# Performance work log

Measured on AMD Instinct MI355X. Metric: run time of the kernel, lower is better.

## Reference

```python
import jax, jax.numpy as jnp
import numpy as np

N, C, H, W = 4, 256, 64, 64
K = 4096

def setup_inputs() -> dict:
    key = jax.random.key(0)
    ks = jax.random.split(key, 9)
    bound = 1.0 / np.sqrt(C)  # torch Linear default init scale
    inp = {
        "latent0": jax.random.normal(ks[0], (N, C, H, W), dtype=jnp.float32),
        "code0": jax.random.randint(ks[1], (N, H, W), 0, K, dtype=jnp.int32).astype(jnp.int64),
        "codebook0": jax.random.normal(ks[2], (K, C), dtype=jnp.float32) * np.sqrt(2.0 / C),  # kaiming-ish
        "Wq": jax.random.uniform(ks[3], (C, C), jnp.float32, -bound, bound),
        "bq": jax.random.uniform(ks[4], (C,), jnp.float32, -bound, bound),
        "Wk": jax.random.uniform(ks[5], (C, C), jnp.float32, -bound, bound),
        "bk": jax.random.uniform(ks[6], (C,), jnp.float32, -bound, bound),
        "Wv": jax.random.uniform(ks[7], (C, C), jnp.float32, -bound, bound),
        "bv": jax.random.uniform(ks[8], (C,), jnp.float32, -bound, bound),
    }
    return inp

def reference(latent0, code0, codebook0, Wq, bq, Wk, bk, Wv, bv):
    n, c, h, w = latent0.shape
    k = codebook0.shape[0]
    scale = jnp.asarray(np.sqrt(k), latent0.dtype)  # NOTE: sqrt(num codewords), per original
    # (n,c,h,w) -> (h*w, n, c) token layout, as in forward()
    x = latent0.transpose(2, 3, 0, 1).reshape(h * w, n, c)
    query = x @ Wq.T + bq                      # (hw, n, c)
    keyp = codebook0 @ Wk.T + bk               # (k, c)
    value = codebook0 @ Wv.T + bv              # (k, c)
    logit = jnp.einsum('snc,kc->snk', query, keyp) / scale  # (hw, n, k)
    code = code0.reshape(n, -1).T              # (hw, n)
    # one_hot @ value == direct gather
    quantized = value[code]                    # (hw, n, c)
    logp = jax.nn.log_softmax(logit, axis=-1)
    negLogP = -jnp.take_along_axis(logp, code[..., None], axis=-1).squeeze(-1).sum(axis=0)  # (n,)
    logit_out = logit.transpose(1, 2, 0).reshape(n, k, h, w)
    quant_out = quantized.transpose(1, 2, 0).reshape(n, c, h, w)
    return (quant_out, logit_out, negLogP)
```

## Files before the change

kernel.cpp:

```cpp
#include <hip/hip_runtime.h>


typedef __attribute__((ext_vector_type(8))) short short8;
typedef __attribute__((ext_vector_type(4))) float f32x4;

__device__ __forceinline__ unsigned short f2bf(float f) {
  unsigned u = __float_as_uint(f);
  u += 0x7fffu + ((u >> 16) & 1u);
  return (unsigned short)(u >> 16);
}
__device__ __forceinline__ float bf2f(unsigned short h) {
  return __uint_as_float(((unsigned)h) << 16);
}
__device__ __forceinline__ void gl_lds16(const void* g, void* l) {
  __builtin_amdgcn_global_load_lds(
      (const __attribute__((address_space(1))) unsigned int*)g,
      (__attribute__((address_space(3))) unsigned int*)l, 16, 0, 0);
}

__global__ __launch_bounds__(256) void ka_trans_pre(
    const float* __restrict__ latent, unsigned short* __restrict__ lt,
    const float* __restrict__ Wq, const float* __restrict__ bq,
    const float* __restrict__ Wk, const float* __restrict__ bk,
    float* __restrict__ WKQT, float* __restrict__ bkq,
    float* __restrict__ wkb, float* __restrict__ bkb) {
  __shared__ __align__(16) float sm[32 * 33 + 8];
  const int bid = blockIdx.x, t = threadIdx.x;
  if (bid < 4096) {
    float(*tile)[33] = (float(*)[33])sm;
    const int n = bid >> 10, ct = (bid >> 7) & 7, st = bid & 127;
    const int x = t & 31, y0 = t >> 5;
    const float* src = latent + ((size_t)n * 256 + ct * 32) * 4096 + st * 32;
#pragma unroll
    for (int p = 0; p < 4; ++p) {
      int cy = y0 + p * 8;
      tile[x][cy] = src[(size_t)cy * 4096 + x];
    }
    __syncthreads();
    unsigned short* dst = lt + ((size_t)n * 4096 + st * 32) * 256 + ct * 32;
#pragma unroll
    for (int p = 0; p < 4; ++p) {
      int sy = y0 + p * 8;
      dst[(size_t)sy * 256 + x] = f2bf(tile[sy][x]);
    }
    return;
  }
  float* red = sm;
  const int idx = bid - 4096;
  if (idx < 256) {
    const int c1 = idx;
    float acc = 0.f;
    for (int c = 0; c < 256; ++c) acc += Wk[c * 256 + t] * Wq[c * 256 + c1];
    WKQT[c1 * 256 + t] = acc;
    float v = bk[t] * Wq[t * 256 + c1];
#pragma unroll
    for (int m = 32; m >= 1; m >>= 1) v += __shfl_xor(v, m);
    if ((t & 63) == 0) red[t >> 6] = v;
    __syncthreads();
    if (t == 0) bkq[c1] = red[0] + red[1] + red[2] + red[3];
  } else {
    float acc = 0.f;
    for (int c = 0; c < 256; ++c) acc += Wk[c * 256 + t] * bq[c];
    wkb[t] = acc;
    float v = bk[t] * bq[t];
#pragma unroll
    for (int m = 32; m >= 1; m >>= 1) v += __shfl_xor(v, m);
    if ((t & 63) == 0) red[t >> 6] = v;
    __syncthreads();
    if (t == 0) bkb[0] = red[0] + red[1] + red[2] + red[3];
  }
}

template <bool OUT_BF16>
__device__ __forceinline__ void gemm_body(char* smem, const float* __restrict__ A,
                                          const float* __restrict__ Bt,
                                          const float* __restrict__ bias,
                                          void* __restrict__ outv, float scale,
                                          int bm, int bn, int t) {
  const int lane = t & 63, wave = t >> 6;
  const int wr = wave >> 1, wc = wave & 1;
  const int l15 = lane & 15, lg = lane >> 4;
  f32x4 acc[4][2] = {};

  for (int kk = 0; kk < 4; ++kk) {
    if (kk) __syncthreads();
#pragma unroll
    for (int i = 0; i < 4; ++i) {
      int p = i * 256 + t;
      int row = p >> 3, cg = p & 7;
      const float* src = A + (bm * 128 + row) * 256 + kk * 64 + cg * 8;
      short8 hi, lo;
#pragma unroll
      for (int j = 0; j < 8; ++j) {
        float x = src[j];
        unsigned short h = f2bf(x);
        hi[j] = (short)h;
        lo[j] = (short)f2bf(x - bf2f(h));
      }
      int dst = (row * 64 + ((cg ^ (row & 7)) * 8)) * 2;
      *(short8*)(smem + dst) = hi;
      *(short8*)(smem + 16384 + dst) = lo;
    }
#pragma unroll
    for (int i = 0; i < 2; ++i) {
      int p = i * 256 + t;
      int row = p >> 3, cg = p & 7;
      const float* src = Bt + (bn * 64 + row) * 256 + kk * 64 + cg * 8;
      short8 hi, lo;
#pragma unroll
      for (int j = 0; j < 8; ++j) {
        float x = src[j];
        unsigned short h = f2bf(x);
        hi[j] = (short)h;
        lo[j] = (short)f2bf(x - bf2f(h));
      }
      int dst = (row * 64 + ((cg ^ (row & 7)) * 8)) * 2;
      *(short8*)(smem + 32768 + dst) = hi;
      *(short8*)(smem + 40960 + dst) = lo;
    }
    __syncthreads();
#pragma unroll
    for (int kk2 = 0; kk2 < 2; ++kk2) {
      short8 ah[4], al[4], bh[2], bl[2];
#pragma unroll
      for (int mi = 0; mi < 4; ++mi) {
        int ra = wr * 64 + mi * 16 + l15;
        int ca = (kk2 * 4 + lg) ^ (ra & 7);
        ah[mi] = *(const short8*)(smem + ra * 128 + ca * 16);
        al[mi] = *(const short8*)(smem + 16384 + ra * 128 + ca * 16);
      }
#pragma unroll
      for (int ni = 0; ni < 2; ++ni) {
        int rb = wc * 32 + ni * 16 + l15;
        int cb = (kk2 * 4 + lg) ^ (rb & 7);
        bh[ni] = *(const short8*)(smem + 32768 + rb * 128 + cb * 16);
        bl[ni] = *(const short8*)(smem + 40960 + rb * 128 + cb * 16);
      }
#pragma unroll
      for (int mi = 0; mi < 4; ++mi)
#pragma unroll
        for (int ni = 0; ni < 2; ++ni) {
          acc[mi][ni] = __builtin_amdgcn_mfma_f32_16x16x32_bf16(ah[mi], bh[ni], acc[mi][ni], 0, 0, 0);
          acc[mi][ni] = __builtin_amdgcn_mfma_f32_16x16x32_bf16(ah[mi], bl[ni], acc[mi][ni], 0, 0, 0);
          acc[mi][ni] = __builtin_amdgcn_mfma_f32_16x16x32_bf16(al[mi], bh[ni], acc[mi][ni], 0, 0, 0);
        }
    }
  }
#pragma unroll
  for (int mi = 0; mi < 4; ++mi) {
    int gk = bm * 128 + wr * 64 + mi * 16 + lg * 4;
#pragma unroll
    for (int ni = 0; ni < 2; ++ni) {
      int gc = bn * 64 + wc * 32 + ni * 16 + l15;
      float bv_ = bias[gc];
#pragma unroll
      for (int e = 0; e < 4; ++e) {
        float v = (acc[mi][ni][e] + bv_) * scale;
        int idx = (gk + e) * 256 + gc;
        if (OUT_BF16)
          ((unsigned short*)outv)[idx] = f2bf(v);
        else
          ((float*)outv)[idx] = v;
      }
    }
  }
}

__global__ __launch_bounds__(256) void kb_weights(
    const float* __restrict__ cb, const float* __restrict__ Wv,
    const float* __restrict__ bv, float* __restrict__ VALUE,
    const float* __restrict__ WKQT, const float* __restrict__ BKQ,
    unsigned short* __restrict__ KWQ, const float* __restrict__ WKB,
    const float* __restrict__ BKB, float* __restrict__ KB) {
  __shared__ __align__(16) char smem[49152];
  const int bid = blockIdx.x, t = threadIdx.x;
  if (bid < 128) {
    gemm_body<false>(smem, cb, Wv, bv, (void*)VALUE, 1.0f, bid >> 2, bid & 3, t);
  } else if (bid < 256) {
    int b = bid - 128;
    gemm_body<true>(smem, cb, WKQT, BKQ, (void*)KWQ, 0.015625f, b >> 2, b & 3, t);
  } else {
    const int l32 = t & 31, r = t >> 5;
    const int row = (bid - 256) * 8 + r;
    float acc = 0.f;
#pragma unroll
    for (int j = 0; j < 8; ++j) {
      int c = l32 + j * 32;
      acc += cb[row * 256 + c] * WKB[c];
    }
#pragma unroll
    for (int m = 16; m >= 1; m >>= 1) acc += __shfl_xor(acc, m);
    if (l32 == 0) KB[row] = (acc + BKB[0]) * 0.015625f;
  }
}

__global__ __launch_bounds__(256) void kc_logit_gather(
    const unsigned short* __restrict__ kwq, const unsigned short* __restrict__ lt,
    const float* __restrict__ kb, float* __restrict__ logit_out,
    float* __restrict__ part, const int* __restrict__ code,
    const float* __restrict__ value, float* __restrict__ outq) {
  __shared__ __align__(16) char smem[34816];
  const int bid0 = blockIdx.x, t = threadIdx.x;
  const int lane = t & 63, wave = t >> 6;

  if (bid0 < 512) {
    float* vt = (float*)smem;
    int* codes = (int*)(smem + 32896);
    const int n = bid0 >> 7, s0 = (bid0 & 127) * 32;
    if (t < 32) codes[t] = code[(n << 12) + s0 + t];
    __syncthreads();
#pragma unroll
    for (int j = 0; j < 8; ++j) {
      int jj = wave * 8 + j;
      int idx = codes[jj];
      f32x4 v = *(const f32x4*)(value + (size_t)idx * 256 + lane * 4);
      float* d = vt + jj * 257 + lane * 4;
      d[0] = v[0]; d[1] = v[1]; d[2] = v[2]; d[3] = v[3];
    }
    __syncthreads();
    const int sl = t & 31, cg = t >> 5;
#pragma unroll
    for (int ci = 0; ci < 32; ++ci) {
      int c = ci * 8 + cg;
      __builtin_nontemporal_store(vt[sl * 257 + c],
                                  outq + (((size_t)(n * 256 + c)) << 12) + s0 + sl);
    }
    return;
  }

  const int bid = bid0 - 512;
  const int xcd = bid & 7, idx = bid >> 3;
  const int wg = xcd * 512 + idx;
  const int n = wg >> 10, rr = wg & 1023, kt = rr >> 5, st = rr & 31;
  const int wr = wave >> 1, wc = wave & 1, l15 = lane & 15, lg = lane >> 4;
  f32x4 acc[4][4] = {};
  const unsigned short* abase = kwq + (size_t)kt * 128 * 256;
  const unsigned short* bbase = lt + ((size_t)n * 4096 + st * 128) * 256;

  auto stage = [&](int kk) {
#pragma unroll
    for (int i = 0; i < 4; ++i) {
      int p0 = (i * 4 + wave) * 64;
      int p = p0 + lane;
      int row = p >> 3, cl = p & 7;
      int goff = row * 256 + kk * 64 + ((cl ^ (row & 7)) * 8);
      gl_lds16(abase + goff, smem + p0 * 16);
      gl_lds16(bbase + goff, smem + 16384 + p0 * 16);
    }
  };

  stage(0);
  for (int kk = 0; kk < 4; ++kk) {
    __syncthreads();
#pragma unroll
    for (int kk2 = 0; kk2 < 2; ++kk2) {
      short8 af[4], bfr[4];
#pragma unroll
      for (int mi = 0; mi < 4; ++mi) {
        int ra = wr * 64 + mi * 16 + l15;
        int ca = (kk2 * 4 + lg) ^ (ra & 7);
        af[mi] = *(const short8*)(smem + ra * 128 + ca * 16);
      }
#pragma unroll
      for (int ni = 0; ni < 4; ++ni) {
        int rb = wc * 64 + ni * 16 + l15;
        int cb = (kk2 * 4 + lg) ^ (rb & 7);
        bfr[ni] = *(const short8*)(smem + 16384 + rb * 128 + cb * 16);
      }
#pragma unroll
      for (int mi = 0; mi < 4; ++mi)
#pragma unroll
        for (int ni = 0; ni < 4; ++ni)
          acc[mi][ni] = __builtin_amdgcn_mfma_f32_16x16x32_bf16(af[mi], bfr[ni], acc[mi][ni], 0, 0, 0);
    }
    if (kk < 3) {
      __syncthreads();
      stage(kk + 1);
    }
  }

  float colsum[4] = {0.f, 0.f, 0.f, 0.f};
  float* lbase = logit_out + (size_t)(n * 4096 + kt * 128) * 4096 + st * 128;
#pragma unroll
  for (int mi = 0; mi < 4; ++mi) {
    int rk = wr * 64 + mi * 16 + lg * 4;
    f32x4 kbv = *(const f32x4*)(kb + kt * 128 + rk);
#pragma unroll
    for (int ni = 0; ni < 4; ++ni) {
      int cs = wc * 64 + ni * 16 + l15;
      float* op = lbase + (size_t)rk * 4096 + cs;
#pragma unroll
      for (int e = 0; e < 4; ++e) {
        float v = acc[mi][ni][e] + kbv[e];
        __builtin_nontemporal_store(v, op + (size_t)e * 4096);
        colsum[ni] += __expf(v);
      }
    }
  }
#pragma unroll
  for (int ni = 0; ni < 4; ++ni) {
    colsum[ni] += __shfl_xor(colsum[ni], 16);
    colsum[ni] += __shfl_xor(colsum[ni], 32);
  }
  float* sums = (float*)(smem + 32768);
  if (lane < 16) {
#pragma unroll
    for (int ni = 0; ni < 4; ++ni)
      sums[wr * 128 + wc * 64 + ni * 16 + lane] = colsum[ni];
  }
  __syncthreads();
  if (t < 128) {
    float tot = sums[t] + sums[128 + t];
    part[((size_t)(n * 32 + kt) << 12) + st * 128 + t] = tot;
  }
}

__global__ __launch_bounds__(256) void kd_nlp(const float* __restrict__ part,
                                              const float* __restrict__ logit,
                                              const int* __restrict__ code,
                                              double* __restrict__ part2) {
  const int bid = blockIdx.x, t = threadIdx.x;
  const int n = bid >> 4;
  const int s = ((bid & 15) << 8) + t;
  float se = 0.f;
#pragma unroll
  for (int kt = 0; kt < 32; ++kt) se += part[((size_t)(n * 32 + kt) << 12) + s];
  int cc = code[(n << 12) + s];
  float lc = logit[((size_t)(n * 4096 + cc) << 12) + s];
  double a = (double)logf(se) - (double)lc;
#pragma unroll
  for (int m = 32; m >= 1; m >>= 1) a += __shfl_xor(a, m);
  __shared__ double red[4];
  if ((t & 63) == 0) red[t >> 6] = a;
  __syncthreads();
  if (t == 0) part2[bid] = red[0] + red[1] + red[2] + red[3];
}

__global__ __launch_bounds__(64) void ke_final(const double* __restrict__ part2,
                                               float* __restrict__ outn) {
  const int t = threadIdx.x;
  const int n = t >> 4, i = t & 15;
  double v = part2[n * 16 + i];
#pragma unroll
  for (int m = 8; m >= 1; m >>= 1) v += __shfl_xor(v, m);
  if (i == 0) outn[n] = (float)v;
}

extern "C" void kernel_launch(void* const* d_in, const int* in_sizes, int n_in,
                              void* d_out, int out_size, void* d_ws, size_t ws_size,
                              hipStream_t stream) {
  const float* latent = (const float*)d_in[0];
  const int* code = (const int*)d_in[1];
  const float* cb = (const float*)d_in[2];
  const float* Wq = (const float*)d_in[3];
  const float* bq = (const float*)d_in[4];
  const float* Wk = (const float*)d_in[5];
  const float* bk = (const float*)d_in[6];
  const float* Wv = (const float*)d_in[7];
  const float* bv = (const float*)d_in[8];

  float* out = (float*)d_out;
  float* outq = out;
  float* outl = out + 4194304;
  float* outn = out + 71303168;

  char* ws = (char*)d_ws;
  unsigned short* LT = (unsigned short*)(ws + 0);
  unsigned short* KWQ = (unsigned short*)(ws + 8388608);
  float* KB = (float*)(ws + 10485760);
  float* VALUE = (float*)(ws + 10502144);
  float* PART = (float*)(ws + 14696448);
  float* WKQT = (float*)(ws + 16793600);
  float* BKQ = (float*)(ws + 17055744);
  float* WKB = (float*)(ws + 17056768);
  float* BKB = (float*)(ws + 17057792);
  double* PART2 = (double*)(ws + 17058816);

  ka_trans_pre<<<4353, 256, 0, stream>>>(latent, LT, Wq, bq, Wk, bk, WKQT, BKQ, WKB, BKB);
  kb_weights<<<768, 256, 0, stream>>>(cb, Wv, bv, VALUE, WKQT, BKQ, KWQ, WKB, BKB, KB);
  kc_logit_gather<<<4608, 256, 0, stream>>>(KWQ, LT, KB, outl, PART, code, VALUE, outq);
  kd_nlp<<<64, 256, 0, stream>>>(PART, outl, code, PART2);
  ke_final<<<1, 64, 0, stream>>>(PART2, outn);
}
```

Before: 113.6 us.

## Transpose MFMA operands for vectorized logit stores; move value GEMM earlier

Swaps the MFMA A/B operands in the logit kernel so each lane holds four consecutive spatial positions for one codeword. The epilogue can then write the logit output as 16-byte vector stores instead of scalar strided nontemporal stores, with column sums reduced across lanes through shuffles. Separately, the codebook-value GEMM moves from the weights kernel into the first transpose/precompute kernel, so it runs alongside the transpose and the weights kernel gets shorter. The larger shared-memory allocation in the first kernel may lower occupancy for the transpose blocks, and the stores lose their nontemporal hint.

Result: slower. 122.8 us (+8.1%).

```diff
diff --git a/kernel.cpp b/kernel.cpp
--- a/kernel.cpp
+++ b/kernel.cpp
@@ -16,59 +16,6 @@
   __builtin_amdgcn_global_load_lds(
       (const __attribute__((address_space(1))) unsigned int*)g,
       (__attribute__((address_space(3))) unsigned int*)l, 16, 0, 0);
-}
-
-__global__ __launch_bounds__(256) void ka_trans_pre(
-    const float* __restrict__ latent, unsigned short* __restrict__ lt,
-    const float* __restrict__ Wq, const float* __restrict__ bq,
-    const float* __restrict__ Wk, const float* __restrict__ bk,
-    float* __restrict__ WKQT, float* __restrict__ bkq,
-    float* __restrict__ wkb, float* __restrict__ bkb) {
-  __shared__ __align__(16) float sm[32 * 33 + 8];
-  const int bid = blockIdx.x, t = threadIdx.x;
-  if (bid < 4096) {
-    float(*tile)[33] = (float(*)[33])sm;
-    const int n = bid >> 10, ct = (bid >> 7) & 7, st = bid & 127;
-    const int x = t & 31, y0 = t >> 5;
-    const float* src = latent + ((size_t)n * 256 + ct * 32) * 4096 + st * 32;
-#pragma unroll
-    for (int p = 0; p < 4; ++p) {
-      int cy = y0 + p * 8;
-      tile[x][cy] = src[(size_t)cy * 4096 + x];
-    }
-    __syncthreads();
-    unsigned short* dst = lt + ((size_t)n * 4096 + st * 32) * 256 + ct * 32;
-#pragma unroll
-    for (int p = 0; p < 4; ++p) {
-      int sy = y0 + p * 8;
-      dst[(size_t)sy * 256 + x] = f2bf(tile[sy][x]);
-    }
-    return;
-  }
-  float* red = sm;
-  const int idx = bid - 4096;
-  if (idx < 256) {
-    const int c1 = idx;
-    float acc = 0.f;
-    for (int c = 0; c < 256; ++c) acc += Wk[c * 256 + t] * Wq[c * 256 + c1];
-    WKQT[c1 * 256 + t] = acc;
-    float v = bk[t] * Wq[t * 256 + c1];
-#pragma unroll
-    for (int m = 32; m >= 1; m >>= 1) v += __shfl_xor(v, m);
-    if ((t & 63) == 0) red[t >> 6] = v;
-    __syncthreads();
-    if (t == 0) bkq[c1] = red[0] + red[1] + red[2] + red[3];
-  } else {
-    float acc = 0.f;
-    for (int c = 0; c < 256; ++c) acc += Wk[c * 256 + t] * bq[c];
-    wkb[t] = acc;
-    float v = bk[t] * bq[t];
-#pragma unroll
-    for (int m = 32; m >= 1; m >>= 1) v += __shfl_xor(v, m);
-    if ((t & 63) == 0) red[t >> 6] = v;
-    __syncthreads();
-    if (t == 0) bkb[0] = red[0] + red[1] + red[2] + red[3];
-  }
 }
 
 template <bool OUT_BF16>
@@ -166,22 +113,77 @@
   }
 }
 
+__global__ __launch_bounds__(256) void ka_trans_pre(
+    const float* __restrict__ latent, unsigned short* __restrict__ lt,
+    const float* __restrict__ Wq, const float* __restrict__ bq,
+    const float* __restrict__ Wk, const float* __restrict__ bk,
+    float* __restrict__ WKQT, float* __restrict__ bkq,
+    float* __restrict__ wkb, float* __restrict__ bkb,
+    const float* __restrict__ cb, const float* __restrict__ Wv,
+    const float* __restrict__ bv, float* __restrict__ VALUE) {
+  __shared__ __align__(16) char smem[49152];
+  const int bid = blockIdx.x, t = threadIdx.x;
+  if (bid < 4096) {
+    float(*tile)[33] = (float(*)[33])smem;
+    const int n = bid >> 10, ct = (bid >> 7) & 7, st = bid & 127;
+    const int x = t & 31, y0 = t >> 5;
+    const float* src = latent + ((size_t)n * 256 + ct * 32) * 4096 + st * 32;
+#pragma unroll
+    for (int p = 0; p < 4; ++p) {
+      int cy = y0 + p * 8;
+      tile[x][cy] = src[(size_t)cy * 4096 + x];
+    }
+    __syncthreads();
+    unsigned short* dst = lt + ((size_t)n * 4096 + st * 32) * 256 + ct * 32;
+#pragma unroll
+    for (int p = 0; p < 4; ++p) {
+      int sy = y0 + p * 8;
+      dst[(size_t)sy * 256 + x] = f2bf(tile[sy][x]);
+    }
+    return;
+  }
+  if (bid < 4224) {
+    int b = bid - 4096;
+    gemm_body<false>(smem, cb, Wv, bv, (void*)VALUE, 1.0f, b >> 2, b & 3, t);
+    return;
+  }
+  float* red = (float*)smem;
+  if (bid < 4480) {
+    const int c1 = bid - 4224;
+    float acc = 0.f;
+    for (int c = 0; c < 256; ++c) acc += Wk[c * 256 + t] * Wq[c * 256 + c1];
+    WKQT[c1 * 256 + t] = acc;
+    float v = bk[t] * Wq[t * 256 + c1];
+#pragma unroll
+    for (int m = 32; m >= 1; m >>= 1) v += __shfl_xor(v, m);
+    if ((t & 63) == 0) red[t >> 6] = v;
+    __syncthreads();
+    if (t == 0) bkq[c1] = red[0] + red[1] + red[2] + red[3];
+  } else {
+    float acc = 0.f;
+    for (int c = 0; c < 256; ++c) acc += Wk[c * 256 + t] * bq[c];
+    wkb[t] = acc;
+    float v = bk[t] * bq[t];
+#pragma unroll
+    for (int m = 32; m >= 1; m >>= 1) v += __shfl_xor(v, m);
+    if ((t & 63) == 0) red[t >> 6] = v;
+    __syncthreads();
+    if (t == 0) bkb[0] = red[0] + red[1] + red[2] + red[3];
+  }
+}
+
 __global__ __launch_bounds__(256) void kb_weights(
-    const float* __restrict__ cb, const float* __restrict__ Wv,
-    const float* __restrict__ bv, float* __restrict__ VALUE,
-    const float* __restrict__ WKQT, const float* __restrict__ BKQ,
-    unsigned short* __restrict__ KWQ, const float* __restrict__ WKB,
-    const float* __restrict__ BKB, float* __restrict__ KB) {
+    const float* __restrict__ cb, const float* __restrict__ WKQT,
+    const float* __restrict__ BKQ, unsigned short* __restrict__ KWQ,
+    const float* __restrict__ WKB, const float* __restrict__ BKB,
+    float* __restrict__ KB) {
   __shared__ __align__(16) char smem[49152];
   const int bid = blockIdx.x, t = threadIdx.x;
   if (bid < 128) {
-    gemm_body<false>(smem, cb, Wv, bv, (void*)VALUE, 1.0f, bid >> 2, bid & 3, t);
-  } else if (bid < 256) {
-    int b = bid - 128;
-    gemm_body<true>(smem, cb, WKQT, BKQ, (void*)KWQ, 0.015625f, b >> 2, b & 3, t);
+    gemm_body<true>(smem, cb, WKQT, BKQ, (void*)KWQ, 0.015625f, bid >> 2, bid & 3, t);
   } else {
     const int l32 = t & 31, r = t >> 5;
-    const int row = (bid - 256) * 8 + r;
+    const int row = (bid - 128) * 8 + r;
     float acc = 0.f;
 #pragma unroll
     for (int j = 0; j < 8; ++j) {
@@ -271,7 +273,7 @@
       for (int mi = 0; mi < 4; ++mi)
 #pragma unroll
         for (int ni = 0; ni < 4; ++ni)
-          acc[mi][ni] = __builtin_amdgcn_mfma_f32_16x16x32_bf16(af[mi], bfr[ni], acc[mi][ni], 0, 0, 0);
+          acc[mi][ni] = __builtin_amdgcn_mfma_f32_16x16x32_bf16(bfr[ni], af[mi], acc[mi][ni], 0, 0, 0);
     }
     if (kk < 3) {
       __syncthreads();
@@ -279,34 +281,38 @@
     }
   }
 
-  float colsum[4] = {0.f, 0.f, 0.f, 0.f};
-  float* lbase = logit_out + (size_t)(n * 4096 + kt * 128) * 4096 + st * 128;
+  f32x4 csum[4] = {};
+  const int sbase = st * 128 + wc * 64;
 #pragma unroll
   for (int mi = 0; mi < 4; ++mi) {
-    int rk = wr * 64 + mi * 16 + lg * 4;
-    f32x4 kbv = *(const f32x4*)(kb + kt * 128 + rk);
+    int gk = kt * 128 + wr * 64 + mi * 16 + l15;
+    float kbv = kb[gk];
+    float* rowp = logit_out + (((size_t)(n * 4096 + gk)) << 12) + sbase + lg * 4;
 #pragma unroll
     for (int ni = 0; ni < 4; ++ni) {
-      int cs = wc * 64 + ni * 16 + l15;
-      float* op = lbase + (size_t)rk * 4096 + cs;
-#pragma unroll
-      for (int e = 0; e < 4; ++e) {
-        float v = acc[mi][ni][e] + kbv[e];
-        __builtin_nontemporal_store(v, op + (size_t)e * 4096);
-        colsum[ni] += __expf(v);
-      }
-    }
-  }
-#pragma unroll
-  for (int ni = 0; ni < 4; ++ni) {
-    colsum[ni] += __shfl_xor(colsum[ni], 16);
-    colsum[ni] += __shfl_xor(colsum[ni], 32);
-  }
+      f32x4 v = acc[mi][ni];
+      v[0] += kbv; v[1] += kbv; v[2] += kbv; v[3] += kbv;
+      *(f32x4*)(rowp + ni * 16) = v;
+      csum[ni][0] += __expf(v[0]);
+      csum[ni][1] += __expf(v[1]);
+      csum[ni][2] += __expf(v[2]);
+      csum[ni][3] += __expf(v[3]);
+    }
+  }
+#pragma unroll
+  for (int ni = 0; ni < 4; ++ni)
+#pragma unroll
+    for (int m = 1; m <= 8; m <<= 1) {
+      csum[ni][0] += __shfl_xor(csum[ni][0], m);
+      csum[ni][1] += __shfl_xor(csum[ni][1], m);
+      csum[ni][2] += __shfl_xor(csum[ni][2], m);
+      csum[ni][3] += __shfl_xor(csum[ni][3], m);
+    }
   float* sums = (float*)(smem + 32768);
-  if (lane < 16) {
+  if (l15 == 0) {
 #pragma unroll
     for (int ni = 0; ni < 4; ++ni)
-      sums[wr * 128 + wc * 64 + ni * 16 + lane] = colsum[ni];
+      *(f32x4*)(sums + wr * 128 + wc * 64 + ni * 16 + lg * 4) = csum[ni];
   }
   __syncthreads();
   if (t < 128) {
@@ -376,8 +382,9 @@
   float* BKB = (float*)(ws + 17057792);
   double* PART2 = (double*)(ws + 17058816);
 
-  ka_trans_pre<<<4353, 256, 0, stream>>>(latent, LT, Wq, bq, Wk, bk, WKQT, BKQ, WKB, BKB);
-  kb_weights<<<768, 256, 0, stream>>>(cb, Wv, bv, VALUE, WKQT, BKQ, KWQ, WKB, BKB, KB);
+  ka_trans_pre<<<4481, 256, 0, stream>>>(latent, LT, Wq, bq, Wk, bk, WKQT, BKQ,
+                                         WKB, BKB, cb, Wv, bv, VALUE);
+  kb_weights<<<640, 256, 0, stream>>>(cb, WKQT, BKQ, KWQ, WKB, BKB, KB);
   kc_logit_gather<<<4608, 256, 0, stream>>>(KWQ, LT, KB, outl, PART, code, VALUE, outq);
   kd_nlp<<<64, 256, 0, stream>>>(PART, outl, code, PART2);
   ke_final<<<1, 64, 0, stream>>>(PART2, outn);
```
